# Performance work log

Measured on AMD Instinct MI355X. Metric: run time of the kernel, lower is better.

Reference implementation:

```python
import jax, jax.numpy as jnp
import numpy as np

EMBED = 256
HEADS = 8
LEVELS = 1
POINTS = 4
NBQ = 2          # num_bev_queue
HBEV = 128
WBEV = 128
BS = 1


def setup_inputs() -> dict:
    key = jax.random.key(0)
    ks = jax.random.split(key, 10)
    Nq = HBEV * WBEV
    E = EMBED
    so_out = NBQ * HEADS * LEVELS * POINTS * 2
    aw_out = NBQ * HEADS * LEVELS * POINTS
    return {
        "query": jax.random.normal(ks[0], (BS, Nq, E), jnp.float32),
        "value": jax.random.normal(ks[1], (BS, NBQ * Nq, E), jnp.float32),
        "reference_points": jax.random.uniform(ks[2], (BS, Nq, LEVELS, 2), jnp.float32),
        # params stored as [in, out]; y = x @ W + b (math-equivalent to torch Linear)
        "W_vproj": jax.random.normal(ks[3], (E, E), jnp.float32) / np.sqrt(E).astype(np.float32),
        "b_vproj": jnp.zeros((E,), jnp.float32),
        "W_so": jax.random.normal(ks[4], (NBQ * E, so_out), jnp.float32) * 0.01,
        "b_so": jax.random.normal(ks[5], (so_out,), jnp.float32) * 0.5,
        "W_aw": jax.random.normal(ks[6], (NBQ * E, aw_out), jnp.float32) * 0.01,
        "b_aw": jnp.zeros((aw_out,), jnp.float32),
        "W_out": jax.random.normal(ks[7], (E, E), jnp.float32) / np.sqrt(E).astype(np.float32),
        "b_out": jnp.zeros((E,), jnp.float32),
        "spatial_shapes": jnp.array([[HBEV, WBEV]], jnp.int32),
        "level_start_index": jnp.array([0], jnp.int32),
    }


def _msda(value, spatial_shapes, sampling_locations, attention_weights):
    """Multi-scale deformable attention (grid_sample semantics: bilinear,
    zero padding, align_corners=False).
    value: [B, sum(H*W), Hh, d]; sampling_locations: [B, Nq, Hh, L, P, 2] in [0,1];
    attention_weights: [B, Nq, Hh, L, P]. Returns [B, Nq, Hh*d]."""
    B, _, Hh, d = value.shape
    _, Nq, _, L, P, _ = sampling_locations.shape
    ss = np.asarray(spatial_shapes)
    out = jnp.zeros((B, Nq, Hh, d), value.dtype)
    start = 0
    for l in range(L):
        H_, W_ = int(ss[l, 0]), int(ss[l, 1])
        v = value[:, start:start + H_ * W_]          # [B, H*W, Hh, d]
        start += H_ * W_
        loc = sampling_locations[:, :, :, l]          # [B, Nq, Hh, P, 2]
        # align_corners=False: pixel = loc*size - 0.5
        px = loc[..., 0] * W_ - 0.5
        py = loc[..., 1] * H_ - 0.5
        x0f = jnp.floor(px)
        y0f = jnp.floor(py)
        lx = px - x0f
        ly = py - y0f
        x0 = x0f.astype(jnp.int32)
        y0 = y0f.astype(jnp.int32)

        def gather(ix, iy):
            valid = ((ix >= 0) & (ix < W_) & (iy >= 0) & (iy < H_))
            idx = jnp.clip(iy, 0, H_ - 1) * W_ + jnp.clip(ix, 0, W_ - 1)   # [B,Nq,Hh,P]
            idx = jnp.transpose(idx, (0, 1, 3, 2)).reshape(B, Nq * P, Hh, 1)
            g = jnp.take_along_axis(v, idx, axis=1).reshape(B, Nq, P, Hh, d)
            m = jnp.transpose(valid, (0, 1, 3, 2))[..., None].astype(value.dtype)
            return g * m

        def wmul(w):  # [B,Nq,Hh,P] -> [B,Nq,P,Hh,1]
            return jnp.transpose(w, (0, 1, 3, 2))[..., None]

        sampled = (wmul((1 - lx) * (1 - ly)) * gather(x0, y0)
                   + wmul(lx * (1 - ly)) * gather(x0 + 1, y0)
                   + wmul((1 - lx) * ly) * gather(x0, y0 + 1)
                   + wmul(lx * ly) * gather(x0 + 1, y0 + 1))   # [B,Nq,P,Hh,d]
        out = out + jnp.einsum('bqphd,bqhp->bqhd', sampled, attention_weights[:, :, :, l])
    return out.reshape(B, Nq, Hh * d)


def reference(query, value, reference_points, W_vproj, b_vproj, W_so, b_so,
              W_aw, b_aw, W_out, b_out, spatial_shapes, level_start_index):
    bs, Nq, E = query.shape
    Hh, L, P, nbq = HEADS, LEVELS, POINTS, NBQ
    identity = query
    # query enhanced with the previous-BEV slice of value
    qe = jnp.concatenate([value[:, :Nq], query], axis=-1)        # [bs, Nq, 2E]
    v = (value @ W_vproj + b_vproj).reshape(bs * nbq, Nq, Hh, E // Hh)
    so = (qe @ W_so + b_so).reshape(bs, Nq, Hh, nbq, L, P, 2)
    aw = jax.nn.softmax((qe @ W_aw + b_aw).reshape(bs, Nq, Hh, nbq, L * P), axis=-1)
    aw = aw.reshape(bs, Nq, Hh, nbq, L, P)
    aw = jnp.transpose(aw, (0, 3, 1, 2, 4, 5)).reshape(bs * nbq, Nq, Hh, L, P)
    so = jnp.transpose(so, (0, 3, 1, 2, 4, 5, 6)).reshape(bs * nbq, Nq, Hh, L, P, 2)
    rp = jnp.tile(reference_points, (nbq, 1, 1, 1))              # [bs*nbq, Nq, L, 2]
    ssf = spatial_shapes.astype(so.dtype)
    offset_normalizer = jnp.stack([ssf[:, 1], ssf[:, 0]], -1)    # [L, 2] = (W, H)
    loc = rp[:, :, None, :, None, :] + so / offset_normalizer[None, None, None, :, None, :]
    out = _msda(v, spatial_shapes, loc, aw).reshape(bs, nbq, Nq, E).mean(axis=1)
    out = out @ W_out + b_out
    return out + identity  # dropout is identity in eval mode
```

## Files before the change

### kernel.cpp

```cpp
#include <hip/hip_runtime.h>
#include <math.h>

#define NQ     16384
#define NHEAD  8
#define GW     128
#define GH     128

typedef __attribute__((ext_vector_type(8))) short short8;
typedef __attribute__((ext_vector_type(4))) float f32x4;

static __device__ __forceinline__ unsigned short f2bf(float f) {
    unsigned u = __builtin_bit_cast(unsigned, f);
    u += 0x7FFFu + ((u >> 16) & 1u);
    return (unsigned short)(u >> 16);
}
static __device__ __forceinline__ unsigned pk2(float lo, float hi) {
    return (unsigned)f2bf(lo) | ((unsigned)f2bf(hi) << 16);
}
static __device__ __forceinline__ float bflo(unsigned u) {
    return __builtin_bit_cast(float, u << 16);
}
static __device__ __forceinline__ float bfhi(unsigned u) {
    return __builtin_bit_cast(float, u & 0xffff0000u);
}

__global__ void prep(const float* __restrict__ Wv, const float* __restrict__ Wso,
                     const float* __restrict__ Waw, const float* __restrict__ bso,
                     const float* __restrict__ baw, const float* __restrict__ Wo,
                     unsigned short* __restrict__ WTv, unsigned short* __restrict__ WTso,
                     unsigned short* __restrict__ WTo, float* __restrict__ bias2)
{
    const int n = blockIdx.x;
    const int k = threadIdx.x;
    WTv[n * 256 + k] = f2bf(Wv[(size_t)k * 256 + n]);
    WTo[n * 256 + k] = f2bf(Wo[(size_t)k * 256 + n]);
    float s0, s1;
    if (n < 128)      { s0 = Wso[(size_t)k * 128 + n];       s1 = Wso[(size_t)(k + 256) * 128 + n]; }
    else if (n < 192) { s0 = Waw[(size_t)k * 64 + n - 128];  s1 = Waw[(size_t)(k + 256) * 64 + n - 128]; }
    else              { s0 = 0.f; s1 = 0.f; }
    WTso[(size_t)n * 512 + k]       = f2bf(s0);
    WTso[(size_t)n * 512 + k + 256] = f2bf(s1);
    if (k == 0) bias2[n] = (n < 128) ? bso[n] : ((n < 192) ? baw[n - 128] : 0.f);
}

template<int KTOT, int MODE>
static __device__ __forceinline__ void gemm_body(
    int m0, int n0,
    const float* __restrict__ A1, const float* __restrict__ A2,
    const unsigned short* __restrict__ Abf,
    const unsigned short* __restrict__ WT,
    const float* __restrict__ bias, const float* __restrict__ resid,
    void* __restrict__ Cout,
    unsigned short* As, unsigned short* Bs)
{
    const int tid = threadIdx.x;
    const int w = tid >> 6, lane = tid & 63;
    const int wr = w >> 1, wc = w & 1;
    const int g = lane >> 4, r16 = lane & 15;
    const int arow = tid >> 3, aoc = tid & 7;
    const int NT = KTOT / 64;

    float4 ra[4];
    uint4  rab[2];
    uint4  rb[4];
    f32x4 acc[2][4] = {};

#define LOAD_T(t)                                                               \
    {                                                                           \
        int k0 = (t) * 64;                                                      \
        if (MODE == 2) {                                                        \
            _Pragma("unroll")                                                   \
            for (int i = 0; i < 2; ++i)                                         \
                rab[i] = *(const uint4*)&Abf[(size_t)(m0 + arow + i * 32) * 256 \
                                             + k0 + aoc * 8];                   \
        } else {                                                                \
            const float* Asrc = (KTOT == 512 && k0 >= 256) ? (A2 + (k0 - 256))  \
                                                           : (A1 + k0);         \
            _Pragma("unroll")                                                   \
            for (int i = 0; i < 2; ++i) {                                       \
                const float* p = Asrc + (size_t)(m0 + arow + i * 32) * 256      \
                                 + aoc * 8;                                     \
                ra[i * 2 + 0] = *(const float4*)p;                              \
                ra[i * 2 + 1] = *(const float4*)(p + 4);                        \
            }                                                                   \
        }                                                                       \
        _Pragma("unroll")                                                       \
        for (int i = 0; i < 4; ++i)                                             \
            rb[i] = *(const uint4*)&WT[(size_t)(n0 + arow + i * 32) * KTOT      \
                                       + k0 + aoc * 8];                         \
    }

#define SWZ(row, chunk) (((chunk) ^ ((row) & 7)) * 8)

#define WRITE_T(bufi)                                                           \
    {                                                                           \
        unsigned short* Ab = As + (bufi) * 64 * 64;                             \
        unsigned short* Bb = Bs + (bufi) * 128 * 64;                            \
        if (MODE == 2) {                                                        \
            _Pragma("unroll")                                                   \
            for (int i = 0; i < 2; ++i) {                                       \
                int r = arow + i * 32;                                          \
                *(uint4*)&Ab[r * 64 + SWZ(r, aoc)] = rab[i];                    \
            }                                                                   \
        } else {                                                                \
            _Pragma("unroll")                                                   \
            for (int i = 0; i < 2; ++i) {                                       \
                uint4 wv;                                                       \
                wv.x = pk2(ra[i * 2].x, ra[i * 2].y);                           \
                wv.y = pk2(ra[i * 2].z, ra[i * 2].w);                           \
                wv.z = pk2(ra[i * 2 + 1].x, ra[i * 2 + 1].y);                   \
                wv.w = pk2(ra[i * 2 + 1].z, ra[i * 2 + 1].w);                   \
                int r = arow + i * 32;                                          \
                *(uint4*)&Ab[r * 64 + SWZ(r, aoc)] = wv;                        \
            }                                                                   \
        }                                                                       \
        _Pragma("unroll")                                                       \
        for (int i = 0; i < 4; ++i) {                                           \
            int r = arow + i * 32;                                              \
            *(uint4*)&Bb[r * 64 + SWZ(r, aoc)] = rb[i];                         \
        }                                                                       \
    }

    LOAD_T(0);
    WRITE_T(0);
    __syncthreads();

    for (int t = 0; t < NT; ++t) {
        if (t + 1 < NT) LOAD_T(t + 1);
        const unsigned short* Ab = As + (t & 1) * 64 * 64;
        const unsigned short* Bb = Bs + (t & 1) * 128 * 64;
        #pragma unroll
        for (int kh = 0; kh < 2; ++kh) {
            short8 af[2], bfr[4];
            #pragma unroll
            for (int mi = 0; mi < 2; ++mi) {
                int r = wr * 32 + mi * 16 + r16;
                af[mi] = *(const short8*)&Ab[r * 64 + SWZ(r, kh * 4 + g)];
            }
            #pragma unroll
            for (int nj = 0; nj < 4; ++nj) {
                int r = wc * 64 + nj * 16 + r16;
                bfr[nj] = *(const short8*)&Bb[r * 64 + SWZ(r, kh * 4 + g)];
            }
            #pragma unroll
            for (int mi = 0; mi < 2; ++mi)
                #pragma unroll
                for (int nj = 0; nj < 4; ++nj)
                    acc[mi][nj] = __builtin_amdgcn_mfma_f32_16x16x32_bf16(
                        af[mi], bfr[nj], acc[mi][nj], 0, 0, 0);
        }
        if (t + 1 < NT) WRITE_T((t + 1) & 1);
        __syncthreads();
    }
#undef LOAD_T
#undef WRITE_T
#undef SWZ

    #pragma unroll
    for (int mi = 0; mi < 2; ++mi) {
        int row = m0 + wr * 32 + mi * 16 + g * 4;
        #pragma unroll
        for (int nj = 0; nj < 4; ++nj) {
            int col = n0 + wc * 64 + nj * 16 + r16;
            if (MODE == 1 && col >= 192) continue;
            float bia = bias[col];
            #pragma unroll
            for (int j = 0; j < 4; ++j) {
                float vo = acc[mi][nj][j] + bia;
                if (MODE == 0) {
                    ((unsigned short*)Cout)[(size_t)(row + j) * 256 + col] = f2bf(vo);
                } else if (MODE == 1) {
                    ((float*)Cout)[(size_t)(row + j) * 192 + col] = vo;
                } else {
                    ((float*)Cout)[(size_t)(row + j) * 256 + col] =
                        vo + resid[(size_t)(row + j) * 256 + col];
                }
            }
        }
    }
}

__global__ __launch_bounds__(256)
void gemm_vs(const float* __restrict__ value, const float* __restrict__ query,
             const unsigned short* __restrict__ WTv, const unsigned short* __restrict__ WTso,
             const float* __restrict__ bv, const float* __restrict__ bias2,
             unsigned short* __restrict__ v_out, float* __restrict__ soaw_out)
{
    __shared__ __align__(16) unsigned short As[2 * 64 * 64];
    __shared__ __align__(16) unsigned short Bs[2 * 128 * 64];
    const int bid = blockIdx.x;
    if (bid < 1024) {
        gemm_body<256, 0>((bid >> 1) * 64, (bid & 1) * 128,
                          value, nullptr, nullptr, WTv, bv, nullptr, v_out, As, Bs);
    } else {
        const int b2 = bid - 1024;
        gemm_body<512, 1>((b2 >> 1) * 64, (b2 & 1) * 128,
                          value, query, nullptr, WTso, bias2, nullptr, soaw_out, As, Bs);
    }
}

__global__ __launch_bounds__(256)
void gemm_out(const unsigned short* __restrict__ Abf, const unsigned short* __restrict__ WTo,
              const float* __restrict__ bo, const float* __restrict__ resid,
              float* __restrict__ out)
{
    __shared__ __align__(16) unsigned short As[2 * 64 * 64];
    __shared__ __align__(16) unsigned short Bs[2 * 128 * 64];
    gemm_body<256, 2>((blockIdx.x >> 1) * 64, (blockIdx.x & 1) * 128,
                      nullptr, nullptr, Abf, WTo, bo, resid, out, As, Bs);
}

static __device__ __forceinline__ void acc8(float* acc, float w, uint4 r) {
    acc[0] = fmaf(w, bflo(r.x), acc[0]);
    acc[1] = fmaf(w, bfhi(r.x), acc[1]);
    acc[2] = fmaf(w, bflo(r.y), acc[2]);
    acc[3] = fmaf(w, bfhi(r.y), acc[3]);
    acc[4] = fmaf(w, bflo(r.z), acc[4]);
    acc[5] = fmaf(w, bfhi(r.z), acc[5]);
    acc[6] = fmaf(w, bflo(r.w), acc[6]);
    acc[7] = fmaf(w, bfhi(r.w), acc[7]);
}

__global__ __launch_bounds__(256)
void sampler(const unsigned short* __restrict__ v, const float* __restrict__ soaw,
             const float* __restrict__ rp, unsigned short* __restrict__ outm)
{
    __shared__ float so_s[4][128];
    __shared__ float w_s[4][64];
    __shared__ float rp_s[4][2];

    const int t = threadIdx.x;
    const int bid = blockIdx.x;
    const int q0 = ((bid & 7) * 512 + (bid >> 3)) * 4;

    #pragma unroll
    for (int i = 0; i < 2; ++i) {
        int idx = t + i * 256;
        int qq = idx >> 7, off = idx & 127;
        so_s[qq][off] = soaw[(size_t)(q0 + qq) * 192 + off];
    }
    if (t < 64) {
        int qq = t >> 4, grp = t & 15;
        float4 a4 = *reinterpret_cast<const float4*>(
            &soaw[(size_t)(q0 + qq) * 192 + 128 + grp * 4]);
        float m = fmaxf(fmaxf(a4.x, a4.y), fmaxf(a4.z, a4.w));
        float e0 = __expf(a4.x - m), e1 = __expf(a4.y - m);
        float e2 = __expf(a4.z - m), e3 = __expf(a4.w - m);
        float inv = 1.f / (e0 + e1 + e2 + e3);
        w_s[qq][grp * 4 + 0] = e0 * inv;
        w_s[qq][grp * 4 + 1] = e1 * inv;
        w_s[qq][grp * 4 + 2] = e2 * inv;
        w_s[qq][grp * 4 + 3] = e3 * inv;
    }
    if (t < 8) rp_s[t >> 1][t & 1] = rp[(size_t)(q0 + (t >> 1)) * 2 + (t & 1)];
    __syncthreads();

    const int wq = t >> 6;
    const int q = q0 + wq;
    const int ln = t & 63;
    const int b = ln >> 5;
    const int s = ln & 31;
    const int h = s >> 2, c = s & 3;
    const int sub = h * 64 + c * 16;
    const float rpx = rp_s[wq][0], rpy = rp_s[wq][1];
    const char* vb = (const char*)v + (size_t)b * NQ * 512;
    float acc[8] = {};

    #pragma unroll
    for (int p = 0; p < 4; ++p) {
        float sox = so_s[wq][h * 16 + b * 8 + p * 2 + 0];
        float soy = so_s[wq][h * 16 + b * 8 + p * 2 + 1];
        float wbp = w_s[wq][h * 8 + b * 4 + p];
        float px = (rpx + sox * (1.0f / 128.0f)) * 128.0f - 0.5f;
        float py = (rpy + soy * (1.0f / 128.0f)) * 128.0f - 0.5f;
        float x0f = floorf(px), y0f = floorf(py);
        float lx = px - x0f, ly = py - y0f;
        int x0 = (int)x0f, y0 = (int)y0f;
        int x1 = x0 + 1, y1 = y0 + 1;
        float wx0 = (1.f - lx) * ((x0 >= 0 && x0 < GW) ? 1.f : 0.f);
        float wx1 = lx         * ((x1 >= 0 && x1 < GW) ? 1.f : 0.f);
        float wy0 = (1.f - ly) * ((y0 >= 0 && y0 < GH) ? 1.f : 0.f);
        float wy1 = ly         * ((y1 >= 0 && y1 < GH) ? 1.f : 0.f);
        int x0c = min(max(x0, 0), GW - 1), x1c = min(max(x1, 0), GW - 1);
        int y0c = min(max(y0, 0), GH - 1), y1c = min(max(y1, 0), GH - 1);
        uint4 r00 = *(const uint4*)(vb + ((size_t)(y0c * GW + x0c) * 512 + sub));
        uint4 r10 = *(const uint4*)(vb + ((size_t)(y0c * GW + x1c) * 512 + sub));
        uint4 r01 = *(const uint4*)(vb + ((size_t)(y1c * GW + x0c) * 512 + sub));
        uint4 r11 = *(const uint4*)(vb + ((size_t)(y1c * GW + x1c) * 512 + sub));
        acc8(acc, wbp * wx0 * wy0, r00);
        acc8(acc, wbp * wx1 * wy0, r10);
        acc8(acc, wbp * wx0 * wy1, r01);
        acc8(acc, wbp * wx1 * wy1, r11);
    }

    #pragma unroll
    for (int i = 0; i < 8; ++i) acc[i] += __shfl_xor(acc[i], 32);

    if (b == 0) {
        uint4 o;
        o.x = pk2(0.5f * acc[0], 0.5f * acc[1]);
        o.y = pk2(0.5f * acc[2], 0.5f * acc[3]);
        o.z = pk2(0.5f * acc[4], 0.5f * acc[5]);
        o.w = pk2(0.5f * acc[6], 0.5f * acc[7]);
        *reinterpret_cast<uint4*>((char*)outm + (size_t)q * 512 + sub) = o;
    }
}

extern "C" void kernel_launch(void* const* d_in, const int* in_sizes, int n_in,
                              void* d_out, int out_size, void* d_ws, size_t ws_size,
                              hipStream_t stream)
{
    const float* query   = (const float*)d_in[0];
    const float* value   = (const float*)d_in[1];
    const float* rp      = (const float*)d_in[2];
    const float* W_vproj = (const float*)d_in[3];
    const float* b_vproj = (const float*)d_in[4];
    const float* W_so    = (const float*)d_in[5];
    const float* b_so    = (const float*)d_in[6];
    const float* W_aw    = (const float*)d_in[7];
    const float* b_aw    = (const float*)d_in[8];
    const float* W_out   = (const float*)d_in[9];
    const float* b_out   = (const float*)d_in[10];
    float* out = (float*)d_out;

    char* wp = (char*)d_ws;
    unsigned short* ws_v    = (unsigned short*)wp; wp += (size_t)2 * NQ * 256 * 2;
    float*          ws_soaw = (float*)wp;          wp += (size_t)NQ * 192 * 4;
    unsigned short* ws_mean = (unsigned short*)wp; wp += (size_t)NQ * 256 * 2;
    unsigned short* WTv     = (unsigned short*)wp; wp += 256 * 256 * 2;
    unsigned short* WTso    = (unsigned short*)wp; wp += 256 * 512 * 2;
    unsigned short* WTo     = (unsigned short*)wp; wp += 256 * 256 * 2;
    float*          bias2   = (float*)wp;          wp += 256 * 4;

    prep<<<dim3(256), dim3(256), 0, stream>>>(W_vproj, W_so, W_aw, b_so, b_aw, W_out,
                                              WTv, WTso, WTo, bias2);
    gemm_vs<<<dim3(1536), dim3(256), 0, stream>>>(value, query, WTv, WTso,
                                                  b_vproj, bias2, ws_v, ws_soaw);
    sampler<<<dim3(NQ / 4), dim3(256), 0, stream>>>(ws_v, ws_soaw, rp, ws_mean);
    gemm_out<<<dim3(512), dim3(256), 0, stream>>>(ws_mean, WTo, b_out, query, out);
}
```

Measured before the change: 80.67 us.

## Prefetch two tiles ahead in GEMM and remap block IDs for locality

The GEMM main loop is unrolled by two with two register sets, so global loads for tile t+2 are issued while tile t is computed. This gives more latency hiding at the cost of extra VGPRs. Block indices are also permuted so that each group of 16 consecutive blocks covers 8 row tiles times both column halves. The remap is meant to change which blocks run together, for better L2 reuse of A rows across XCDs or CUs.

New measurement: 108.6 us. 1.35x slower.

```diff
diff --git a/kernel.cpp b/kernel.cpp
--- a/kernel.cpp
+++ b/kernel.cpp
@@ -60,12 +60,12 @@
     const int arow = tid >> 3, aoc = tid & 7;
     const int NT = KTOT / 64;
 
-    float4 ra[4];
-    uint4  rab[2];
-    uint4  rb[4];
+    float4 ra0[4], ra1[4];
+    uint4  rab0[2], rab1[2];
+    uint4  rb0[4], rb1[4];
     f32x4 acc[2][4] = {};
 
-#define LOAD_T(t)                                                               \
+#define LOAD_S(t, ra, rab, rb)                                                  \
     {                                                                           \
         int k0 = (t) * 64;                                                      \
         if (MODE == 2) {                                                        \
@@ -92,7 +92,7 @@
 
 #define SWZ(row, chunk) (((chunk) ^ ((row) & 7)) * 8)
 
-#define WRITE_T(bufi)                                                           \
+#define WRITE_S(bufi, ra, rab, rb)                                              \
     {                                                                           \
         unsigned short* Ab = As + (bufi) * 64 * 64;                             \
         unsigned short* Bb = Bs + (bufi) * 128 * 64;                            \
@@ -121,39 +121,52 @@
         }                                                                       \
     }
 
-    LOAD_T(0);
-    WRITE_T(0);
+#define COMPUTE(bufi)                                                           \
+    {                                                                           \
+        const unsigned short* Ab = As + (bufi) * 64 * 64;                       \
+        const unsigned short* Bb = Bs + (bufi) * 128 * 64;                      \
+        _Pragma("unroll")                                                       \
+        for (int kh = 0; kh < 2; ++kh) {                                        \
+            short8 af[2], bfr[4];                                               \
+            _Pragma("unroll")                                                   \
+            for (int mi = 0; mi < 2; ++mi) {                                    \
+                int r = wr * 32 + mi * 16 + r16;                                \
+                af[mi] = *(const short8*)&Ab[r * 64 + SWZ(r, kh * 4 + g)];      \
+            }                                                                   \
+            _Pragma("unroll")                                                   \
+            for (int nj = 0; nj < 4; ++nj) {                                    \
+                int r = wc * 64 + nj * 16 + r16;                                \
+                bfr[nj] = *(const short8*)&Bb[r * 64 + SWZ(r, kh * 4 + g)];     \
+            }                                                                   \
+            _Pragma("unroll")                                                   \
+            for (int mi = 0; mi < 2; ++mi)                                      \
+                _Pragma("unroll")                                               \
+                for (int nj = 0; nj < 4; ++nj)                                  \
+                    acc[mi][nj] = __builtin_amdgcn_mfma_f32_16x16x32_bf16(      \
+                        af[mi], bfr[nj], acc[mi][nj], 0, 0, 0);                 \
+        }                                                                       \
+    }
+
+    LOAD_S(0, ra0, rab0, rb0);
+    WRITE_S(0, ra0, rab0, rb0);
+    LOAD_S(1, ra1, rab1, rb1);
     __syncthreads();
 
-    for (int t = 0; t < NT; ++t) {
-        if (t + 1 < NT) LOAD_T(t + 1);
-        const unsigned short* Ab = As + (t & 1) * 64 * 64;
-        const unsigned short* Bb = Bs + (t & 1) * 128 * 64;
-        #pragma unroll
-        for (int kh = 0; kh < 2; ++kh) {
-            short8 af[2], bfr[4];
-            #pragma unroll
-            for (int mi = 0; mi < 2; ++mi) {
-                int r = wr * 32 + mi * 16 + r16;
-                af[mi] = *(const short8*)&Ab[r * 64 + SWZ(r, kh * 4 + g)];
-            }
-            #pragma unroll
-            for (int nj = 0; nj < 4; ++nj) {
-                int r = wc * 64 + nj * 16 + r16;
-                bfr[nj] = *(const short8*)&Bb[r * 64 + SWZ(r, kh * 4 + g)];
-            }
-            #pragma unroll
-            for (int mi = 0; mi < 2; ++mi)
-                #pragma unroll
-                for (int nj = 0; nj < 4; ++nj)
-                    acc[mi][nj] = __builtin_amdgcn_mfma_f32_16x16x32_bf16(
-                        af[mi], bfr[nj], acc[mi][nj], 0, 0, 0);
+    for (int t = 0; t < NT; t += 2) {
+        if (t + 2 < NT) LOAD_S(t + 2, ra0, rab0, rb0);
+        COMPUTE(0);
+        if (t + 1 < NT) WRITE_S(1, ra1, rab1, rb1);
+        __syncthreads();
+        if (t + 1 < NT) {
+            if (t + 3 < NT) LOAD_S(t + 3, ra1, rab1, rb1);
+            COMPUTE(1);
+            if (t + 2 < NT) WRITE_S(0, ra0, rab0, rb0);
+            __syncthreads();
         }
-        if (t + 1 < NT) WRITE_T((t + 1) & 1);
-        __syncthreads();
-    }
-#undef LOAD_T
-#undef WRITE_T
+    }
+#undef LOAD_S
+#undef WRITE_S
+#undef COMPUTE
 #undef SWZ
 
     #pragma unroll
@@ -188,12 +201,13 @@
 {
     __shared__ __align__(16) unsigned short As[2 * 64 * 64];
     __shared__ __align__(16) unsigned short Bs[2 * 128 * 64];
-    const int bid = blockIdx.x;
-    if (bid < 1024) {
-        gemm_body<256, 0>((bid >> 1) * 64, (bid & 1) * 128,
+    const int b = blockIdx.x;
+    const int role = ((b >> 4) * 8 + (b & 7)) * 2 + ((b & 15) >> 3);
+    if (role < 1024) {
+        gemm_body<256, 0>((role >> 1) * 64, (role & 1) * 128,
                           value, nullptr, nullptr, WTv, bv, nullptr, v_out, As, Bs);
     } else {
-        const int b2 = bid - 1024;
+        const int b2 = role - 1024;
         gemm_body<512, 1>((b2 >> 1) * 64, (b2 & 1) * 128,
                           value, query, nullptr, WTso, bias2, nullptr, soaw_out, As, Bs);
     }
@@ -206,7 +220,9 @@
 {
     __shared__ __align__(16) unsigned short As[2 * 64 * 64];
     __shared__ __align__(16) unsigned short Bs[2 * 128 * 64];
-    gemm_body<256, 2>((blockIdx.x >> 1) * 64, (blockIdx.x & 1) * 128,
+    const int b = blockIdx.x;
+    const int role = ((b >> 4) * 8 + (b & 7)) * 2 + ((b & 15) >> 3);
+    gemm_body<256, 2>((role >> 1) * 64, (role & 1) * 128,
                       nullptr, nullptr, Abf, WTo, bo, resid, out, As, Bs);
 }
 
```

## Halve GEMM K-tile to 32, add occupancy hint and block remap for reuse

Applied to the files above, without the earlier changes.

Shrinks the GEMM K-step from 64 to 32, which halves shared memory per block and the register staging per thread. The swizzle is adapted to the 32-wide rows. Launch bounds now request 5 blocks per CU to raise occupancy. Block indices are remapped so that consecutive groups of 8 blocks share the same weight column half, which is meant to improve L2 reuse. In exchange there are twice as many barrier iterations and fewer MFMAs between each sync.

New measurement: 90.00 us. 11.6% more time.

```diff
diff --git a/kernel.cpp b/kernel.cpp
--- a/kernel.cpp
+++ b/kernel.cpp
@@ -2,7 +2,6 @@
 #include <math.h>
 
 #define NQ     16384
-#define NHEAD  8
 #define GW     128
 #define GH     128
 
@@ -43,6 +42,8 @@
     if (k == 0) bias2[n] = (n < 128) ? bso[n] : ((n < 192) ? baw[n - 128] : 0.f);
 }
 
+#define SWZ(row, chunk) ((((chunk) ^ (((row) >> 1) & 3))) * 8)
+
 template<int KTOT, int MODE>
 static __device__ __forceinline__ void gemm_body(
     int m0, int n0,
@@ -57,67 +58,51 @@
     const int w = tid >> 6, lane = tid & 63;
     const int wr = w >> 1, wc = w & 1;
     const int g = lane >> 4, r16 = lane & 15;
-    const int arow = tid >> 3, aoc = tid & 7;
-    const int NT = KTOT / 64;
-
-    float4 ra[4];
-    uint4  rab[2];
-    uint4  rb[4];
+    const int arow = tid >> 2, aoc = tid & 3;
+    const int NT = KTOT / 32;
+
+    float4 ra[2];
+    uint4  rab;
+    uint4  rb[2];
     f32x4 acc[2][4] = {};
 
 #define LOAD_T(t)                                                               \
     {                                                                           \
-        int k0 = (t) * 64;                                                      \
+        int k0 = (t) * 32;                                                      \
         if (MODE == 2) {                                                        \
-            _Pragma("unroll")                                                   \
-            for (int i = 0; i < 2; ++i)                                         \
-                rab[i] = *(const uint4*)&Abf[(size_t)(m0 + arow + i * 32) * 256 \
-                                             + k0 + aoc * 8];                   \
+            rab = *(const uint4*)&Abf[(size_t)(m0 + arow) * 256 + k0 + aoc * 8];\
         } else {                                                                \
             const float* Asrc = (KTOT == 512 && k0 >= 256) ? (A2 + (k0 - 256))  \
                                                            : (A1 + k0);         \
-            _Pragma("unroll")                                                   \
-            for (int i = 0; i < 2; ++i) {                                       \
-                const float* p = Asrc + (size_t)(m0 + arow + i * 32) * 256      \
-                                 + aoc * 8;                                     \
-                ra[i * 2 + 0] = *(const float4*)p;                              \
-                ra[i * 2 + 1] = *(const float4*)(p + 4);                        \
-            }                                                                   \
+            const float* p = Asrc + (size_t)(m0 + arow) * 256 + aoc * 8;        \
+            ra[0] = *(const float4*)p;                                          \
+            ra[1] = *(const float4*)(p + 4);                                    \
         }                                                                       \
         _Pragma("unroll")                                                       \
-        for (int i = 0; i < 4; ++i)                                             \
-            rb[i] = *(const uint4*)&WT[(size_t)(n0 + arow + i * 32) * KTOT      \
-                                       + k0 + aoc * 8];                         \
-    }
-
-#define SWZ(row, chunk) (((chunk) ^ ((row) & 7)) * 8)
+        for (int j = 0; j < 2; ++j) {                                           \
+            int id = tid + j * 256;                                             \
+            int r = id >> 2, c = id & 3;                                        \
+            rb[j] = *(const uint4*)&WT[(size_t)(n0 + r) * KTOT + k0 + c * 8];   \
+        }                                                                       \
+    }
 
 #define WRITE_T(bufi)                                                           \
     {                                                                           \
-        unsigned short* Ab = As + (bufi) * 64 * 64;                             \
-        unsigned short* Bb = Bs + (bufi) * 128 * 64;                            \
+        unsigned short* Ab = As + (bufi) * 64 * 32;                             \
+        unsigned short* Bb = Bs + (bufi) * 128 * 32;                            \
         if (MODE == 2) {                                                        \
-            _Pragma("unroll")                                                   \
-            for (int i = 0; i < 2; ++i) {                                       \
-                int r = arow + i * 32;                                          \
-                *(uint4*)&Ab[r * 64 + SWZ(r, aoc)] = rab[i];                    \
-            }                                                                   \
+            *(uint4*)&Ab[arow * 32 + SWZ(arow, aoc)] = rab;                     \
         } else {                                                                \
-            _Pragma("unroll")                                                   \
-            for (int i = 0; i < 2; ++i) {                                       \
-                uint4 wv;                                                       \
-                wv.x = pk2(ra[i * 2].x, ra[i * 2].y);                           \
-                wv.y = pk2(ra[i * 2].z, ra[i * 2].w);                           \
-                wv.z = pk2(ra[i * 2 + 1].x, ra[i * 2 + 1].y);                   \
-                wv.w = pk2(ra[i * 2 + 1].z, ra[i * 2 + 1].w);                   \
-                int r = arow + i * 32;                                          \
-                *(uint4*)&Ab[r * 64 + SWZ(r, aoc)] = wv;                        \
-            }                                                                   \
+            uint4 wv;                                                           \
+            wv.x = pk2(ra[0].x, ra[0].y); wv.y = pk2(ra[0].z, ra[0].w);         \
+            wv.z = pk2(ra[1].x, ra[1].y); wv.w = pk2(ra[1].z, ra[1].w);         \
+            *(uint4*)&Ab[arow * 32 + SWZ(arow, aoc)] = wv;                      \
         }                                                                       \
         _Pragma("unroll")                                                       \
-        for (int i = 0; i < 4; ++i) {                                           \
-            int r = arow + i * 32;                                              \
-            *(uint4*)&Bb[r * 64 + SWZ(r, aoc)] = rb[i];                         \
+        for (int j = 0; j < 2; ++j) {                                           \
+            int id = tid + j * 256;                                             \
+            int r = id >> 2, c = id & 3;                                        \
+            *(uint4*)&Bb[r * 32 + SWZ(r, c)] = rb[j];                           \
         }                                                                       \
     }
 
@@ -127,34 +112,30 @@
 
     for (int t = 0; t < NT; ++t) {
         if (t + 1 < NT) LOAD_T(t + 1);
-        const unsigned short* Ab = As + (t & 1) * 64 * 64;
-        const unsigned short* Bb = Bs + (t & 1) * 128 * 64;
+        const unsigned short* Ab = As + (t & 1) * 64 * 32;
+        const unsigned short* Bb = Bs + (t & 1) * 128 * 32;
+        short8 af[2], bfr[4];
         #pragma unroll
-        for (int kh = 0; kh < 2; ++kh) {
-            short8 af[2], bfr[4];
+        for (int mi = 0; mi < 2; ++mi) {
+            int r = wr * 32 + mi * 16 + r16;
+            af[mi] = *(const short8*)&Ab[r * 32 + SWZ(r, g)];
+        }
+        #pragma unroll
+        for (int nj = 0; nj < 4; ++nj) {
+            int r = wc * 64 + nj * 16 + r16;
+            bfr[nj] = *(const short8*)&Bb[r * 32 + SWZ(r, g)];
+        }
+        #pragma unroll
+        for (int mi = 0; mi < 2; ++mi)
             #pragma unroll
-            for (int mi = 0; mi < 2; ++mi) {
-                int r = wr * 32 + mi * 16 + r16;
-                af[mi] = *(const short8*)&Ab[r * 64 + SWZ(r, kh * 4 + g)];
-            }
-            #pragma unroll
-            for (int nj = 0; nj < 4; ++nj) {
-                int r = wc * 64 + nj * 16 + r16;
-                bfr[nj] = *(const short8*)&Bb[r * 64 + SWZ(r, kh * 4 + g)];
-            }
-            #pragma unroll
-            for (int mi = 0; mi < 2; ++mi)
-                #pragma unroll
-                for (int nj = 0; nj < 4; ++nj)
-                    acc[mi][nj] = __builtin_amdgcn_mfma_f32_16x16x32_bf16(
-                        af[mi], bfr[nj], acc[mi][nj], 0, 0, 0);
-        }
+            for (int nj = 0; nj < 4; ++nj)
+                acc[mi][nj] = __builtin_amdgcn_mfma_f32_16x16x32_bf16(
+                    af[mi], bfr[nj], acc[mi][nj], 0, 0, 0);
         if (t + 1 < NT) WRITE_T((t + 1) & 1);
         __syncthreads();
     }
 #undef LOAD_T
 #undef WRITE_T
-#undef SWZ
 
     #pragma unroll
     for (int mi = 0; mi < 2; ++mi) {
@@ -180,33 +161,37 @@
     }
 }
 
-__global__ __launch_bounds__(256)
+__global__ __launch_bounds__(256, 5)
 void gemm_vs(const float* __restrict__ value, const float* __restrict__ query,
              const unsigned short* __restrict__ WTv, const unsigned short* __restrict__ WTso,
              const float* __restrict__ bv, const float* __restrict__ bias2,
              unsigned short* __restrict__ v_out, float* __restrict__ soaw_out)
 {
-    __shared__ __align__(16) unsigned short As[2 * 64 * 64];
-    __shared__ __align__(16) unsigned short Bs[2 * 128 * 64];
+    __shared__ __align__(16) unsigned short As[2 * 64 * 32];
+    __shared__ __align__(16) unsigned short Bs[2 * 128 * 32];
     const int bid = blockIdx.x;
     if (bid < 1024) {
-        gemm_body<256, 0>((bid >> 1) * 64, (bid & 1) * 128,
+        const int role = ((bid >> 4) * 8 + (bid & 7)) * 2 + ((bid >> 3) & 1);
+        gemm_body<256, 0>((role >> 1) * 64, (role & 1) * 128,
                           value, nullptr, nullptr, WTv, bv, nullptr, v_out, As, Bs);
     } else {
-        const int b2 = bid - 1024;
-        gemm_body<512, 1>((b2 >> 1) * 64, (b2 & 1) * 128,
+        const int j = bid - 1024;
+        const int role = ((j >> 4) * 8 + (j & 7)) * 2 + ((j >> 3) & 1);
+        gemm_body<512, 1>((role >> 1) * 64, (role & 1) * 128,
                           value, query, nullptr, WTso, bias2, nullptr, soaw_out, As, Bs);
     }
 }
 
-__global__ __launch_bounds__(256)
+__global__ __launch_bounds__(256, 5)
 void gemm_out(const unsigned short* __restrict__ Abf, const unsigned short* __restrict__ WTo,
               const float* __restrict__ bo, const float* __restrict__ resid,
               float* __restrict__ out)
 {
-    __shared__ __align__(16) unsigned short As[2 * 64 * 64];
-    __shared__ __align__(16) unsigned short Bs[2 * 128 * 64];
-    gemm_body<256, 2>((blockIdx.x >> 1) * 64, (blockIdx.x & 1) * 128,
+    __shared__ __align__(16) unsigned short As[2 * 64 * 32];
+    __shared__ __align__(16) unsigned short Bs[2 * 128 * 32];
+    const int b = blockIdx.x;
+    const int role = ((b >> 4) * 8 + (b & 7)) * 2 + ((b >> 3) & 1);
+    gemm_body<256, 2>((role >> 1) * 64, (role & 1) * 128,
                       nullptr, nullptr, Abf, WTo, bo, resid, out, As, Bs);
 }
 
```
